# Kernel optimization log

Hardware: AMD Instinct MI355X
Metric: run time of the kernel (lower is better)

The kernel has to match this reference:

```python
import jax, jax.numpy as jnp
import numpy as np
from jax import lax

ALPHA = 0.98
DELTA = 2.0
R = 0.5
S = 0.025
EPS = 1e-6


def setup_inputs() -> dict:
    key = jax.random.key(0)
    # non-negative energy spectrogram [B, n_mels, T]
    x = jax.random.uniform(key, (64, 128, 4000), dtype=jnp.float32)
    return {"x": x}


def _pcen(x):
    # x: [B, C, T]; EMA smoother: smooth[0] = x[0], smooth[t] = (1-s)*smooth[t-1] + s*x[t]
    xt = jnp.moveaxis(x, -1, 0)  # [T, B, C]

    def step(carry, x_t):
        sm = (1.0 - S) * carry + S * x_t
        return sm, sm

    init = xt[0]
    _, sm_rest = lax.scan(step, init, xt[1:])  # [T-1, B, C]
    smooth = jnp.concatenate([init[None], sm_rest], axis=0)  # [T, B, C]
    smooth = jnp.moveaxis(smooth, 0, -1)  # [B, C, T]
    pcen = (x / (smooth + EPS) ** ALPHA + DELTA) ** R - DELTA ** R
    return pcen


def reference(x):
    return _pcen(x)
```

## Files before the change

### kernel.cpp

```cpp
#include <hip/hip_runtime.h>
#include <math.h>


constexpr int   TLEN = 4000;
constexpr int   NF4  = 1000;
constexpr int   NTH  = 256;
constexpr int   HALF = 8;
constexpr float S_C  = 0.025f;
constexpr float A_1  = 1.0f - S_C;

typedef float f4_t __attribute__((ext_vector_type(4)));

constexpr float fpow(float b, int n) {
    float r = 1.0f;
    for (int i = 0; i < n; ++i) r *= b;
    return r;
}
constexpr float A_2  = fpow(A_1, 2);
constexpr float A_3  = fpow(A_1, 3);
constexpr float A256 = fpow(A_1, 256);

constexpr float L2A4 = -0.14610359f;

constexpr float ALPHA = 0.98f;
constexpr float EPS_C = 1e-6f;
constexpr float SQRT2 = 1.41421356237309515f;

__device__ __forceinline__ float pcen_elem(float x, float sm) {
    float t = sm + EPS_C;
    float p = __builtin_amdgcn_exp2f(-ALPHA * __builtin_amdgcn_logf(t));
    float y = fmaf(x, p, 2.0f);
    return __builtin_amdgcn_sqrtf(y) - SQRT2;
}

__device__ __forceinline__ void load_half(f4_t (&v)[HALF], const f4_t* __restrict__ x4,
                                          int lane, int h ) {
#pragma unroll
    for (int j = 0; j < HALF; ++j) {
        const int f4 = lane + 64 * (h * HALF + j);
        v[j] = (f4 < NF4) ? x4[f4] : (f4_t){0.f, 0.f, 0.f, 0.f};
    }
}

__device__ __forceinline__ void compute_half(const f4_t (&v)[HALF], f4_t* __restrict__ o4,
                                             int lane, float Al, float& e,
                                             int h, bool store_ok) {
    constexpr float CD[6] = { fpow(A_1, 4),  fpow(A_1, 8),  fpow(A_1, 16),
                              fpow(A_1, 32), fpow(A_1, 64), fpow(A_1, 128) };
    float B[HALF];
#pragma unroll
    for (int j = 0; j < HALF; ++j) {
        f4_t  r  = v[j];
        float b0 = (h == 0 && j == 0 && lane == 0) ? r.x : S_C * r.x;
        B[j] = fmaf(A_3, b0, S_C * fmaf(A_2, r.y, fmaf(A_1, r.z, r.w)));
    }
#pragma unroll
    for (int s = 0; s < 6; ++s) {
        const int   d  = 1 << s;
        const float cc = CD[s];
        float Bp[HALF];
#pragma unroll
        for (int j = 0; j < HALF; ++j) Bp[j] = __shfl_up(B[j], d);
        const bool ok = (lane >= d);
#pragma unroll
        for (int j = 0; j < HALF; ++j) B[j] = fmaf(cc, ok ? Bp[j] : 0.0f, B[j]);
    }
#pragma unroll
    for (int j = 0; j < HALF; ++j) {
        const int k  = h * HALF + j;
        float Tk = __shfl(B[j], 63);
        float Bi = __shfl_up(B[j], 1);
        if (lane == 0) Bi = 0.0f;
        float sm = fmaf(Al, e, Bi);

        f4_t  r  = v[j];
        float b0 = (h == 0 && j == 0 && lane == 0) ? r.x : S_C * r.x;
        float s0 = fmaf(A_1, sm, b0);
        float s1 = fmaf(A_1, s0, S_C * r.y);
        float s2 = fmaf(A_1, s1, S_C * r.z);
        float s3 = fmaf(A_1, s2, S_C * r.w);

        f4_t o;
        o.x = pcen_elem(r.x, s0);
        o.y = pcen_elem(r.y, s1);
        o.z = pcen_elem(r.z, s2);
        o.w = pcen_elem(r.w, s3);

        const int f4 = lane + 64 * k;
        if (store_ok && f4 < NF4) __builtin_nontemporal_store(o, &o4[f4]);

        e = fmaf(A256, e, Tk);
    }
}

__global__ __launch_bounds__(NTH) void pcen_kernel(const float* __restrict__ x,
                                                   float* __restrict__ out,
                                                   int nch) {
    const int lane = threadIdx.x & 63;
    const int wid  = blockIdx.x * (NTH / 64) + (threadIdx.x >> 6);
    const int nw   = gridDim.x * (NTH / 64);
    const int c0   = wid;
    const int c1   = wid + nw;
    if (c0 >= nch) return;
    const bool has1 = (c1 < nch);

    const f4_t* __restrict__ x0 = (const f4_t*)(x + (size_t)c0 * TLEN);
    const f4_t* __restrict__ x1 = (const f4_t*)(x + (size_t)(has1 ? c1 : c0) * TLEN);
    f4_t*       __restrict__ o0 = (f4_t*)(out + (size_t)c0 * TLEN);
    f4_t*       __restrict__ o1 = (f4_t*)(out + (size_t)(has1 ? c1 : c0) * TLEN);

    const float Al = __builtin_amdgcn_exp2f((float)lane * L2A4);

    f4_t  va[HALF], vb[HALF];
    float e = 0.0f;

    load_half(va, x0, lane, 0);
    __builtin_amdgcn_sched_barrier(0);

    load_half(vb, x0, lane, 1);
    __builtin_amdgcn_sched_barrier(0);
    compute_half(va, o0, lane, Al, e, 0, true);

    load_half(va, x1, lane, 0);
    __builtin_amdgcn_sched_barrier(0);
    compute_half(vb, o0, lane, Al, e, 1, true);

    e = 0.0f;
    load_half(vb, x1, lane, 1);
    __builtin_amdgcn_sched_barrier(0);
    compute_half(va, o1, lane, Al, e, 0, has1);

    compute_half(vb, o1, lane, Al, e, 1, has1);
}

extern "C" void kernel_launch(void* const* d_in, const int* in_sizes, int n_in,
                              void* d_out, int out_size, void* d_ws, size_t ws_size,
                              hipStream_t stream) {
    const float* x   = (const float*)d_in[0];
    float*       out = (float*)d_out;
    const int nch    = in_sizes[0] / TLEN;
    const int wpb    = NTH / 64;
    const int nw     = (nch + 1) / 2;
    const int grid   = (nw + wpb - 1) / wpb;
    pcen_kernel<<<grid, NTH, 0, stream>>>(x, out, nch);
}
```

Baseline: 231.8 us.

## Load input via global_load_lds into shared memory, one channel per wave

Replaces register-based double-buffered loads with direct global-to-LDS asynchronous loads, then reads tiles from LDS into registers. Each wave now handles one channel instead of two, which doubles the grid. Nontemporal stores become plain stores. The aim is to overlap the second half's load with compute on the first and to raise occupancy, at the cost of extra LDS traffic and hand-written waitcnt synchronization.

Result: no change. 228.2 us (-1.6%).

```diff
diff --git a/kernel.cpp b/kernel.cpp
--- a/kernel.cpp
+++ b/kernel.cpp
@@ -33,26 +33,16 @@
     return __builtin_amdgcn_sqrtf(y) - SQRT2;
 }
 
-__device__ __forceinline__ void load_half(f4_t (&v)[HALF], const f4_t* __restrict__ x4,
-                                          int lane, int h ) {
-#pragma unroll
-    for (int j = 0; j < HALF; ++j) {
-        const int f4 = lane + 64 * (h * HALF + j);
-        v[j] = (f4 < NF4) ? x4[f4] : (f4_t){0.f, 0.f, 0.f, 0.f};
-    }
-}
-
-__device__ __forceinline__ void compute_half(const f4_t (&v)[HALF], f4_t* __restrict__ o4,
-                                             int lane, float Al, float& e,
-                                             int h, bool store_ok) {
+template <int H>
+__device__ __forceinline__ void compute_half(const f4_t (&r)[HALF], f4_t* __restrict__ o4,
+                                             int lane, float Al, float& e) {
     constexpr float CD[6] = { fpow(A_1, 4),  fpow(A_1, 8),  fpow(A_1, 16),
                               fpow(A_1, 32), fpow(A_1, 64), fpow(A_1, 128) };
     float B[HALF];
 #pragma unroll
     for (int j = 0; j < HALF; ++j) {
-        f4_t  r  = v[j];
-        float b0 = (h == 0 && j == 0 && lane == 0) ? r.x : S_C * r.x;
-        B[j] = fmaf(A_3, b0, S_C * fmaf(A_2, r.y, fmaf(A_1, r.z, r.w)));
+        float b0 = (H == 0 && j == 0 && lane == 0) ? r[j].x : S_C * r[j].x;
+        B[j] = fmaf(A_3, b0, S_C * fmaf(A_2, r[j].y, fmaf(A_1, r[j].z, r[j].w)));
     }
 #pragma unroll
     for (int s = 0; s < 6; ++s) {
@@ -67,27 +57,26 @@
     }
 #pragma unroll
     for (int j = 0; j < HALF; ++j) {
-        const int k  = h * HALF + j;
+        const int k  = H * HALF + j;
         float Tk = __shfl(B[j], 63);
         float Bi = __shfl_up(B[j], 1);
         if (lane == 0) Bi = 0.0f;
         float sm = fmaf(Al, e, Bi);
 
-        f4_t  r  = v[j];
-        float b0 = (h == 0 && j == 0 && lane == 0) ? r.x : S_C * r.x;
+        float b0 = (H == 0 && j == 0 && lane == 0) ? r[j].x : S_C * r[j].x;
         float s0 = fmaf(A_1, sm, b0);
-        float s1 = fmaf(A_1, s0, S_C * r.y);
-        float s2 = fmaf(A_1, s1, S_C * r.z);
-        float s3 = fmaf(A_1, s2, S_C * r.w);
+        float s1 = fmaf(A_1, s0, S_C * r[j].y);
+        float s2 = fmaf(A_1, s1, S_C * r[j].z);
+        float s3 = fmaf(A_1, s2, S_C * r[j].w);
 
         f4_t o;
-        o.x = pcen_elem(r.x, s0);
-        o.y = pcen_elem(r.y, s1);
-        o.z = pcen_elem(r.z, s2);
-        o.w = pcen_elem(r.w, s3);
+        o.x = pcen_elem(r[j].x, s0);
+        o.y = pcen_elem(r[j].y, s1);
+        o.z = pcen_elem(r[j].z, s2);
+        o.w = pcen_elem(r[j].w, s3);
 
         const int f4 = lane + 64 * k;
-        if (store_ok && f4 < NF4) __builtin_nontemporal_store(o, &o4[f4]);
+        if (f4 < NF4) o4[f4] = o;
 
         e = fmaf(A256, e, Tk);
     }
@@ -96,41 +85,57 @@
 __global__ __launch_bounds__(NTH) void pcen_kernel(const float* __restrict__ x,
                                                    float* __restrict__ out,
                                                    int nch) {
+    __shared__ f4_t lds[NTH / 64][HALF][64];
     const int lane = threadIdx.x & 63;
-    const int wid  = blockIdx.x * (NTH / 64) + (threadIdx.x >> 6);
-    const int nw   = gridDim.x * (NTH / 64);
-    const int c0   = wid;
-    const int c1   = wid + nw;
-    if (c0 >= nch) return;
-    const bool has1 = (c1 < nch);
+    const int wv   = threadIdx.x >> 6;
+    const int ch   = blockIdx.x * (NTH / 64) + wv;
+    if (ch >= nch) return;
 
-    const f4_t* __restrict__ x0 = (const f4_t*)(x + (size_t)c0 * TLEN);
-    const f4_t* __restrict__ x1 = (const f4_t*)(x + (size_t)(has1 ? c1 : c0) * TLEN);
-    f4_t*       __restrict__ o0 = (f4_t*)(out + (size_t)c0 * TLEN);
-    f4_t*       __restrict__ o1 = (f4_t*)(out + (size_t)(has1 ? c1 : c0) * TLEN);
+    const f4_t* __restrict__ x4 = (const f4_t*)(x + (size_t)ch * TLEN);
+    f4_t*       __restrict__ o4 = (f4_t*)(out + (size_t)ch * TLEN);
+
+#pragma unroll
+    for (int j = 0; j < HALF; ++j) {
+        const f4_t* src = x4 + (64 * j + lane);
+        __builtin_amdgcn_global_load_lds(
+            (const __attribute__((address_space(1))) void*)src,
+            (__attribute__((address_space(3))) void*)&lds[wv][j][0], 16, 0, 0);
+    }
 
     const float Al = __builtin_amdgcn_exp2f((float)lane * L2A4);
-
-    f4_t  va[HALF], vb[HALF];
     float e = 0.0f;
 
-    load_half(va, x0, lane, 0);
+    asm volatile("s_waitcnt vmcnt(0)" ::: "memory");
+    __builtin_amdgcn_sched_barrier(0);
+    f4_t r0[HALF];
+#pragma unroll
+    for (int j = 0; j < HALF; ++j) r0[j] = lds[wv][j][lane];
+    asm volatile("s_waitcnt lgkmcnt(0)" ::: "memory");
     __builtin_amdgcn_sched_barrier(0);
 
-    load_half(vb, x0, lane, 1);
+#pragma unroll
+    for (int j = 0; j < HALF; ++j) {
+        int f4i = 64 * (HALF + j) + lane;
+        int idx = (f4i < NF4) ? f4i : (NF4 - 1);
+        const f4_t* src = x4 + idx;
+        __builtin_amdgcn_global_load_lds(
+            (const __attribute__((address_space(1))) void*)src,
+            (__attribute__((address_space(3))) void*)&lds[wv][j][0], 16, 0, 0);
+    }
     __builtin_amdgcn_sched_barrier(0);
-    compute_half(va, o0, lane, Al, e, 0, true);
 
-    load_half(va, x1, lane, 0);
+    compute_half<0>(r0, o4, lane, Al, e);
+
+    asm volatile("s_waitcnt vmcnt(8)" ::: "memory");
     __builtin_amdgcn_sched_barrier(0);
-    compute_half(vb, o0, lane, Al, e, 1, true);
-
-    e = 0.0f;
-    load_half(vb, x1, lane, 1);
-    __builtin_amdgcn_sched_barrier(0);
-    compute_half(va, o1, lane, Al, e, 0, has1);
-
-    compute_half(vb, o1, lane, Al, e, 1, has1);
+    f4_t r1[HALF];
+#pragma unroll
+    for (int j = 0; j < HALF; ++j) {
+        r1[j] = lds[wv][j][lane];
+        const int f4i = 64 * (HALF + j) + lane;
+        if (f4i >= NF4) r1[j] = (f4_t){0.f, 0.f, 0.f, 0.f};
+    }
+    compute_half<1>(r1, o4, lane, Al, e);
 }
 
 extern "C" void kernel_launch(void* const* d_in, const int* in_sizes, int n_in,
@@ -140,7 +145,6 @@
     float*       out = (float*)d_out;
     const int nch    = in_sizes[0] / TLEN;
     const int wpb    = NTH / 64;
-    const int nw     = (nch + 1) / 2;
-    const int grid   = (nw + wpb - 1) / wpb;
+    const int grid   = (nch + wpb - 1) / wpb;
     pcen_kernel<<<grid, NTH, 0, stream>>>(x, out, nch);
 }
```
